# Kernel optimization log

Measured on AMD Instinct MI355X. Metric: run time of the kernel, lower is better.

Reference implementation:

```python
import jax, jax.numpy as jnp
import numpy as np

D = 1024
H = 16
HD = D // H
EPS = 1e-5


def layer_norm(x, g, b):
    mu = jnp.mean(x, axis=-1, keepdims=True)
    var = jnp.mean((x - mu) ** 2, axis=-1, keepdims=True)
    return (x - mu) * jax.lax.rsqrt(var + EPS) * g + b


def setup_inputs() -> dict:
    key = jax.random.key(0)
    ks = jax.random.split(key, 10)
    s = lambda fan_in: 1.0 / np.sqrt(fan_in)
    inp = {
        "x": jax.random.normal(ks[0], (2, 2048, D), dtype=jnp.float32),
        "w_qkv": jax.random.uniform(ks[1], (D, 3 * D), minval=-s(D), maxval=s(D)),
        "b_qkv": jnp.zeros((3 * D,), jnp.float32),
        "w_fc": jax.random.uniform(ks[2], (D, D), minval=-s(D), maxval=s(D)),
        "b_fc": jnp.zeros((D,), jnp.float32),
        "ln1_g": jnp.ones((D,), jnp.float32),
        "ln1_b": jnp.zeros((D,), jnp.float32),
        "ln2_g": jnp.ones((D,), jnp.float32),
        "ln2_b": jnp.zeros((D,), jnp.float32),
        "w1": jax.random.uniform(ks[3], (D, 4 * D), minval=-s(D), maxval=s(D)),
        "b1": jnp.zeros((4 * D,), jnp.float32),
        "w2": jax.random.uniform(ks[4], (4 * D, D), minval=-s(4 * D), maxval=s(4 * D)),
        "b2": jnp.zeros((D,), jnp.float32),
    }
    return inp


def reference(x, w_qkv, b_qkv, w_fc, b_fc, ln1_g, ln1_b, ln2_g, ln2_b, w1, b1, w2, b2):
    B, T, C = x.shape
    # --- attention sublayer (pre-norm) ---
    h = layer_norm(x, ln1_g, ln1_b)
    qkv = (h @ w_qkv + b_qkv).reshape(B, T, 3, H, HD)
    q, k, v = qkv[:, :, 0], qkv[:, :, 1], qkv[:, :, 2]  # [B,T,H,HD]
    scores = jnp.einsum("bqhd,bkhd->bhqk", q, k) / np.sqrt(HD).astype(np.float32)
    causal = jnp.tril(jnp.ones((T, T), dtype=bool))
    scores = jnp.where(causal, scores, -jnp.inf)
    weights = jax.nn.softmax(scores, axis=-1)
    out = jnp.einsum("bhqk,bkhd->bqhd", weights, v).reshape(B, T, C)
    x = x + out @ w_fc + b_fc
    # --- MLP sublayer (pre-norm) ---
    h = layer_norm(x, ln2_g, ln2_b)
    h = jax.nn.gelu(h @ w1 + b1, approximate=False) @ w2 + b2
    return x + h
```

## Files before the change

kernel.cpp:

```cpp
#include <hip/hip_runtime.h>
#include <hip/hip_bf16.h>
#include <cstdint>
#include <cstddef>

#define SEQ 2048
#define DM  1024

typedef __attribute__((ext_vector_type(8))) __bf16 bf16x8;
typedef __attribute__((ext_vector_type(4))) float  f32x4;
using bf16 = __hip_bfloat16;

__device__ __forceinline__ void gload_lds16(const bf16* g, bf16* l) {
  __builtin_amdgcn_global_load_lds((const __attribute__((address_space(1))) void*)g,
                                   (__attribute__((address_space(3))) void*)l,
                                   16, 0, 0);
}

__global__ void transpose_to_bf16(const float* __restrict__ in, bf16* __restrict__ out,
                                  int K, int N) {
  __shared__ float tile[32][33];
  const int k0 = blockIdx.y * 32, n0 = blockIdx.x * 32;
  const int tx = threadIdx.x, ty = threadIdx.y;
#pragma unroll
  for (int i = ty; i < 32; i += 8)
    tile[i][tx] = in[(size_t)(k0 + i) * N + n0 + tx];
  __syncthreads();
#pragma unroll
  for (int i = ty; i < 32; i += 8)
    out[(size_t)(n0 + i) * K + k0 + tx] = __float2bfloat16(tile[tx][i]);
}

__global__ void ln_to_bf16(const float* __restrict__ x, const float* __restrict__ g,
                           const float* __restrict__ bt, bf16* __restrict__ out) {
  const int row = blockIdx.x;
  const float4 v = ((const float4*)(x + (size_t)row * DM))[threadIdx.x];
  float s  = v.x + v.y + v.z + v.w;
  float s2 = v.x * v.x + v.y * v.y + v.z * v.z + v.w * v.w;
#pragma unroll
  for (int o = 32; o > 0; o >>= 1) { s += __shfl_down(s, o); s2 += __shfl_down(s2, o); }
  __shared__ float red[8];
  const int wave = threadIdx.x >> 6, lane = threadIdx.x & 63;
  if (lane == 0) { red[wave] = s; red[4 + wave] = s2; }
  __syncthreads();
  s  = red[0] + red[1] + red[2] + red[3];
  s2 = red[4] + red[5] + red[6] + red[7];
  const float mu  = s * (1.f / DM);
  const float var = s2 * (1.f / DM) - mu * mu;
  const float r   = rsqrtf(var + 1e-5f);
  const float4 gv = ((const float4*)g)[threadIdx.x];
  const float4 bv = ((const float4*)bt)[threadIdx.x];
  bf16* o = out + (size_t)row * DM + threadIdx.x * 4;
  o[0] = __float2bfloat16((v.x - mu) * r * gv.x + bv.x);
  o[1] = __float2bfloat16((v.y - mu) * r * gv.y + bv.y);
  o[2] = __float2bfloat16((v.z - mu) * r * gv.z + bv.z);
  o[3] = __float2bfloat16((v.w - mu) * r * gv.w + bv.w);
}

enum { EP_BF16 = 0, EP_GELU = 1, EP_RESID = 2 };

template <int MODE>
__global__ void gemm_bt(const bf16* __restrict__ A, const bf16* __restrict__ Bt,
                        const float* __restrict__ bias, const float* __restrict__ resid,
                        float* __restrict__ Cf, bf16* __restrict__ Cb,
                        int M, int N, int K) {
  __shared__ __attribute__((aligned(16))) bf16 As[128 * 32];
  __shared__ __attribute__((aligned(16))) bf16 Bs[128 * 32];
  const int tid  = threadIdx.x;
  const int wave = tid >> 6, lane = tid & 63;
  const int l16 = lane & 15, lq = lane >> 4;
  const int m0 = blockIdx.x * 128, n0 = blockIdx.y * 128;
  const int wr = (wave >> 1) * 64, wc = (wave & 1) * 64;

  f32x4 acc[4][4];
#pragma unroll
  for (int i = 0; i < 4; i++)
#pragma unroll
    for (int j = 0; j < 4; j++) acc[i][j] = 0;

  const int srow = tid >> 2;
  const int scol = (tid & 3) * 8;
  const bf16* ga = A  + (size_t)(m0 + srow) * K + scol;
  const bf16* gb = Bt + (size_t)(n0 + srow) * K + scol;
  bf16* la = As + (size_t)wave * 512;
  bf16* lb = Bs + (size_t)wave * 512;

  for (int kt = 0; kt < K; kt += 32) {
    gload_lds16(ga + kt, la);
    gload_lds16(ga + (size_t)64 * K + kt, la + 2048);
    gload_lds16(gb + kt, lb);
    gload_lds16(gb + (size_t)64 * K + kt, lb + 2048);
    __syncthreads();
    bf16x8 af[4], bfr[4];
#pragma unroll
    for (int mi = 0; mi < 4; mi++)
      af[mi] = *(const bf16x8*)(As + (wr + mi * 16 + l16) * 32 + lq * 8);
#pragma unroll
    for (int ni = 0; ni < 4; ni++)
      bfr[ni] = *(const bf16x8*)(Bs + (wc + ni * 16 + l16) * 32 + lq * 8);
#pragma unroll
    for (int mi = 0; mi < 4; mi++)
#pragma unroll
      for (int ni = 0; ni < 4; ni++)
        acc[mi][ni] = __builtin_amdgcn_mfma_f32_16x16x32_bf16(af[mi], bfr[ni], acc[mi][ni], 0, 0, 0);
    __syncthreads();
  }

#pragma unroll
  for (int ni = 0; ni < 4; ni++) {
    const int col = n0 + wc + ni * 16 + l16;
    const float bb = bias[col];
#pragma unroll
    for (int mi = 0; mi < 4; mi++) {
#pragma unroll
      for (int r = 0; r < 4; r++) {
        const int row = m0 + wr + mi * 16 + lq * 4 + r;
        const size_t idx = (size_t)row * N + col;
        float v = acc[mi][ni][r] + bb;
        if (MODE == EP_BF16) {
          Cb[idx] = __float2bfloat16(v);
        } else if (MODE == EP_GELU) {
          v = 0.5f * v * (1.0f + erff(v * 0.70710678118654752f));
          Cb[idx] = __float2bfloat16(v);
        } else {
          Cf[idx] = resid[idx] + v;
        }
      }
    }
  }
}

#define SCALE_LOG2 0.18033688011112042f

__global__ void flash_attn(const bf16* __restrict__ qkv, bf16* __restrict__ out) {
  const int id = blockIdx.x;
  const int a  = id & 7;
  const int h  = (id >> 3) & 15;
  const int b  = (id >> 7) & 1;
  const int m  = (id >> 8) & 3;
  const int qb = a ^ (((m & 1) * 15) | ((m & 2) << 3));

  const int tid = threadIdx.x;
  const int w = tid >> 6, lane = tid & 63;
  const int l16 = lane & 15, lq = lane >> 4;

  const size_t base = (size_t)b * SEQ * 3072;
  const bf16* Qg = qkv + base + (size_t)h * 64;
  const bf16* Kg = qkv + base + 1024 + (size_t)h * 64;
  const ushort* Vg = (const ushort*)(qkv + base + 2048 + (size_t)h * 64);

  __shared__ __attribute__((aligned(16))) bf16 Qs[64][72];
  __shared__ __attribute__((aligned(16))) bf16 Ks[64][72];
  __shared__ __attribute__((aligned(16))) bf16 VTs[64 * 64];
  __shared__ __attribute__((aligned(16))) bf16 Ps[4][16][72];

  const int q0 = qb * 64;
  const int nkb = qb + 1;

  const int krow = tid >> 2, kcol = (tid & 3) * 16;
  const int vd = tid & 63, vc = tid >> 6;
  const int vsw0 = ((vc ^ (vd & 7)) * 8);
  const int vsw1 = (((vc + 4) ^ (vd & 7)) * 8);

  {
    const int r = tid >> 2, c = (tid & 3) * 16;
    const bf16* src = Qg + (size_t)(q0 + r) * 3072 + c;
    *(uint4*)(&Qs[r][c])     = *(const uint4*)(src);
    *(uint4*)(&Qs[r][c + 8]) = *(const uint4*)(src + 8);

    const bf16* ks = Kg + (size_t)krow * 3072 + kcol;
    const uint4 k0 = *(const uint4*)(ks);
    const uint4 k1 = *(const uint4*)(ks + 8);
    ushort va[8], vb[8];
#pragma unroll
    for (int j = 0; j < 8; j++) va[j] = Vg[(size_t)(vc * 8 + j) * 3072 + vd];
#pragma unroll
    for (int j = 0; j < 8; j++) vb[j] = Vg[(size_t)((vc + 4) * 8 + j) * 3072 + vd];
    *(uint4*)(&Ks[krow][kcol])     = k0;
    *(uint4*)(&Ks[krow][kcol + 8]) = k1;
    uint4 wa, wb;
    wa.x = (uint)va[0] | ((uint)va[1] << 16); wa.y = (uint)va[2] | ((uint)va[3] << 16);
    wa.z = (uint)va[4] | ((uint)va[5] << 16); wa.w = (uint)va[6] | ((uint)va[7] << 16);
    wb.x = (uint)vb[0] | ((uint)vb[1] << 16); wb.y = (uint)vb[2] | ((uint)vb[3] << 16);
    wb.z = (uint)vb[4] | ((uint)vb[5] << 16); wb.w = (uint)vb[6] | ((uint)vb[7] << 16);
    *(uint4*)(&VTs[vd * 64 + vsw0]) = wa;
    *(uint4*)(&VTs[vd * 64 + vsw1]) = wb;
  }
  __syncthreads();

  const bf16x8 qf0 = *(const bf16x8*)(&Qs[w * 16 + l16][lq * 8]);
  const bf16x8 qf1 = *(const bf16x8*)(&Qs[w * 16 + l16][32 + lq * 8]);

  f32x4 oacc[4];
#pragma unroll
  for (int i = 0; i < 4; i++) oacc[i] = 0;
  float lsum[4] = {0.f, 0.f, 0.f, 0.f};

  uint4 kr0, kr1;
  ushort va[8], vb[8];
  const int sw0 = (lq ^ (l16 & 7)) * 8;
  const int sw1 = ((4 + lq) ^ (l16 & 7)) * 8;

  for (int kb = 0; kb < nkb; ++kb) {
    const bool more = (kb + 1 < nkb);

    if (more) {
      const size_t koff = (size_t)((kb + 1) * 64);
      const bf16* ks = Kg + (koff + krow) * 3072 + kcol;
      kr0 = *(const uint4*)(ks);
      kr1 = *(const uint4*)(ks + 8);
#pragma unroll
      for (int j = 0; j < 8; j++) va[j] = Vg[(koff + vc * 8 + j) * 3072 + vd];
#pragma unroll
      for (int j = 0; j < 8; j++) vb[j] = Vg[(koff + (vc + 4) * 8 + j) * 3072 + vd];
    }

    f32x4 sacc[4];
#pragma unroll
    for (int nt = 0; nt < 4; nt++) sacc[nt] = 0;
#pragma unroll
    for (int nt = 0; nt < 4; nt++) {
      const bf16x8 kf0 = *(const bf16x8*)(&Ks[nt * 16 + l16][lq * 8]);
      const bf16x8 kf1 = *(const bf16x8*)(&Ks[nt * 16 + l16][32 + lq * 8]);
      sacc[nt] = __builtin_amdgcn_mfma_f32_16x16x32_bf16(qf0, kf0, sacc[nt], 0, 0, 0);
      sacc[nt] = __builtin_amdgcn_mfma_f32_16x16x32_bf16(qf1, kf1, sacc[nt], 0, 0, 0);
    }

    const bool diag = (kb == qb);
#pragma unroll
    for (int r = 0; r < 4; r++) {
      float e[4];
#pragma unroll
      for (int nt = 0; nt < 4; nt++) {
        float sv = sacc[nt][r] * SCALE_LOG2;
        sv = fminf(sv, 88.f);
        if (diag && (nt * 16 + l16 > w * 16 + lq * 4 + r)) sv = -1e30f;
        e[nt] = exp2f(sv);
        Ps[w][lq * 4 + r][nt * 16 + l16] = __float2bfloat16(e[nt]);
      }
      lsum[r] += (e[0] + e[1]) + (e[2] + e[3]);
    }

    const bf16x8 pf0 = *(const bf16x8*)(&Ps[w][l16][lq * 8]);
    const bf16x8 pf1 = *(const bf16x8*)(&Ps[w][l16][32 + lq * 8]);
#pragma unroll
    for (int dt = 0; dt < 4; dt++) {
      const int d = dt * 16 + l16;
      const bf16x8 vf0 = *(const bf16x8*)(&VTs[d * 64 + sw0]);
      const bf16x8 vf1 = *(const bf16x8*)(&VTs[d * 64 + sw1]);
      oacc[dt] = __builtin_amdgcn_mfma_f32_16x16x32_bf16(pf0, vf0, oacc[dt], 0, 0, 0);
      oacc[dt] = __builtin_amdgcn_mfma_f32_16x16x32_bf16(pf1, vf1, oacc[dt], 0, 0, 0);
    }

    if (more) {
      __syncthreads();
      *(uint4*)(&Ks[krow][kcol])     = kr0;
      *(uint4*)(&Ks[krow][kcol + 8]) = kr1;
      uint4 wa, wb;
      wa.x = (uint)va[0] | ((uint)va[1] << 16); wa.y = (uint)va[2] | ((uint)va[3] << 16);
      wa.z = (uint)va[4] | ((uint)va[5] << 16); wa.w = (uint)va[6] | ((uint)va[7] << 16);
      wb.x = (uint)vb[0] | ((uint)vb[1] << 16); wb.y = (uint)vb[2] | ((uint)vb[3] << 16);
      wb.z = (uint)vb[4] | ((uint)vb[5] << 16); wb.w = (uint)vb[6] | ((uint)vb[7] << 16);
      *(uint4*)(&VTs[vd * 64 + vsw0]) = wa;
      *(uint4*)(&VTs[vd * 64 + vsw1]) = wb;
      __syncthreads();
    }
  }

#pragma unroll
  for (int r = 0; r < 4; r++) {
    float l = lsum[r];
    l += __shfl_xor(l, 1);
    l += __shfl_xor(l, 2);
    l += __shfl_xor(l, 4);
    l += __shfl_xor(l, 8);
    lsum[r] = 1.f / l;
  }
#pragma unroll
  for (int dt = 0; dt < 4; dt++)
#pragma unroll
    for (int r = 0; r < 4; r++) {
      const int qrow = q0 + w * 16 + lq * 4 + r;
      const float v = oacc[dt][r] * lsum[r];
      out[(size_t)(b * SEQ + qrow) * DM + h * 64 + dt * 16 + l16] = __float2bfloat16(v);
    }
}

extern "C" void kernel_launch(void* const* d_in, const int* in_sizes, int n_in,
                              void* d_out, int out_size, void* d_ws, size_t ws_size,
                              hipStream_t stream) {
  const float* x     = (const float*)d_in[0];
  const float* w_qkv = (const float*)d_in[1];
  const float* b_qkv = (const float*)d_in[2];
  const float* w_fc  = (const float*)d_in[3];
  const float* b_fc  = (const float*)d_in[4];
  const float* ln1_g = (const float*)d_in[5];
  const float* ln1_b = (const float*)d_in[6];
  const float* ln2_g = (const float*)d_in[7];
  const float* ln2_b = (const float*)d_in[8];
  const float* w1    = (const float*)d_in[9];
  const float* b1    = (const float*)d_in[10];
  const float* w2    = (const float*)d_in[11];
  const float* b2    = (const float*)d_in[12];
  float* out = (float*)d_out;

  char* ws    = (char*)d_ws;
  float* x2   = (float*)(ws);
  bf16* big   = (bf16*)(ws + (size_t)(16 << 20));
  bf16* small = (bf16*)(ws + (size_t)(48 << 20));
  bf16* wT    = (bf16*)(ws + (size_t)(56 << 20));

  const dim3 tb(32, 8);

  ln_to_bf16<<<dim3(4096), dim3(256), 0, stream>>>(x, ln1_g, ln1_b, small);
  transpose_to_bf16<<<dim3(96, 32), tb, 0, stream>>>(w_qkv, wT, 1024, 3072);
  gemm_bt<EP_BF16><<<dim3(32, 24), dim3(256), 0, stream>>>(
      small, wT, b_qkv, nullptr, nullptr, big, 4096, 3072, 1024);
  flash_attn<<<dim3(1024), dim3(256), 0, stream>>>(big, small);
  transpose_to_bf16<<<dim3(32, 32), tb, 0, stream>>>(w_fc, wT, 1024, 1024);
  gemm_bt<EP_RESID><<<dim3(32, 8), dim3(256), 0, stream>>>(
      small, wT, b_fc, x, x2, nullptr, 4096, 1024, 1024);
  ln_to_bf16<<<dim3(4096), dim3(256), 0, stream>>>(x2, ln2_g, ln2_b, small);
  transpose_to_bf16<<<dim3(128, 32), tb, 0, stream>>>(w1, wT, 1024, 4096);
  gemm_bt<EP_GELU><<<dim3(32, 32), dim3(256), 0, stream>>>(
      small, wT, b1, nullptr, nullptr, big, 4096, 4096, 1024);
  transpose_to_bf16<<<dim3(32, 128), tb, 0, stream>>>(w2, wT, 4096, 1024);
  gemm_bt<EP_RESID><<<dim3(32, 8), dim3(256), 0, stream>>>(
      big, wT, b2, x2, out, nullptr, 4096, 1024, 4096);
}
```

Before: 412.1 us.

## Register-prefetch GEMM tiles with double-buffered swizzled LDS and one barrier

Replaces the direct global-to-LDS loads in the bf16 GEMM with register prefetch three k-tiles ahead, written into a double-buffered LDS tile. The LDS layout gets an XOR swizzle to reduce bank conflicts on the MFMA fragment reads, and the per-iteration barrier count drops from two to one. The aim is to hide global memory latency behind MFMA work. In exchange it uses more registers (16 uint4 prefetch slots) and twice the LDS, which may lower occupancy.

```diff
diff --git a/kernel.cpp b/kernel.cpp
--- a/kernel.cpp
+++ b/kernel.cpp
@@ -8,13 +8,8 @@
 
 typedef __attribute__((ext_vector_type(8))) __bf16 bf16x8;
 typedef __attribute__((ext_vector_type(4))) float  f32x4;
+using bfl6_dummy = int;
 using bf16 = __hip_bfloat16;
-
-__device__ __forceinline__ void gload_lds16(const bf16* g, bf16* l) {
-  __builtin_amdgcn_global_load_lds((const __attribute__((address_space(1))) void*)g,
-                                   (__attribute__((address_space(3))) void*)l,
-                                   16, 0, 0);
-}
 
 __global__ void transpose_to_bf16(const float* __restrict__ in, bf16* __restrict__ out,
                                   int K, int N) {
@@ -63,8 +58,9 @@
                         const float* __restrict__ bias, const float* __restrict__ resid,
                         float* __restrict__ Cf, bf16* __restrict__ Cb,
                         int M, int N, int K) {
-  __shared__ __attribute__((aligned(16))) bf16 As[128 * 32];
-  __shared__ __attribute__((aligned(16))) bf16 Bs[128 * 32];
+  constexpr int BUF = 128 * 32;
+  __shared__ __attribute__((aligned(16))) bf16 As[2 * BUF];
+  __shared__ __attribute__((aligned(16))) bf16 Bs[2 * BUF];
   const int tid  = threadIdx.x;
   const int wave = tid >> 6, lane = tid & 63;
   const int l16 = lane & 15, lq = lane >> 4;
@@ -78,31 +74,69 @@
     for (int j = 0; j < 4; j++) acc[i][j] = 0;
 
   const int srow = tid >> 2;
-  const int scol = (tid & 3) * 8;
-  const bf16* ga = A  + (size_t)(m0 + srow) * K + scol;
-  const bf16* gb = Bt + (size_t)(n0 + srow) * K + scol;
-  bf16* la = As + (size_t)wave * 512;
-  bf16* lb = Bs + (size_t)wave * 512;
-
-  for (int kt = 0; kt < K; kt += 32) {
-    gload_lds16(ga + kt, la);
-    gload_lds16(ga + (size_t)64 * K + kt, la + 2048);
-    gload_lds16(gb + kt, lb);
-    gload_lds16(gb + (size_t)64 * K + kt, lb + 2048);
+  const int sc   = tid & 3;
+  const int scs  = sc ^ ((srow >> 1) & 3);
+  const bf16* ga = A  + (size_t)(m0 + srow) * K + scs * 8;
+  const bf16* gb = Bt + (size_t)(n0 + srow) * K + scs * 8;
+  const int lw = srow * 32 + sc * 8;
+
+  uint4 pa0[4], pa1[4], pb0[4], pb1[4];
+  const int NKT = K >> 5;
+#pragma unroll
+  for (int p = 0; p < 3; p++) {
+    const int kt = p << 5;
+    pa0[p] = *(const uint4*)(ga + kt);
+    pa1[p] = *(const uint4*)(ga + (size_t)64 * K + kt);
+    pb0[p] = *(const uint4*)(gb + kt);
+    pb1[p] = *(const uint4*)(gb + (size_t)64 * K + kt);
+  }
+  *(uint4*)(As + lw)        = pa0[0];
+  *(uint4*)(As + 2048 + lw) = pa1[0];
+  *(uint4*)(Bs + lw)        = pb0[0];
+  *(uint4*)(Bs + 2048 + lw) = pb1[0];
+
+  int racol[4], rbcol[4];
+#pragma unroll
+  for (int i = 0; i < 4; i++) {
+    const int ra = wr + i * 16 + l16;
+    racol[i] = ra * 32 + (lq ^ ((ra >> 1) & 3)) * 8;
+    const int rb = wc + i * 16 + l16;
+    rbcol[i] = rb * 32 + (lq ^ ((rb >> 1) & 3)) * 8;
+  }
+
+#pragma unroll 4
+  for (int it = 0; it < NKT; ++it) {
     __syncthreads();
+    const int cur = it & 1;
+    if (it + 1 < NKT) {
+      const int s = (it + 1) & 3;
+      bf16* Ad = As + (cur ^ 1) * BUF + lw;
+      bf16* Bd = Bs + (cur ^ 1) * BUF + lw;
+      *(uint4*)(Ad)        = pa0[s];
+      *(uint4*)(Ad + 2048) = pa1[s];
+      *(uint4*)(Bd)        = pb0[s];
+      *(uint4*)(Bd + 2048) = pb1[s];
+    }
+    if (it + 3 < NKT) {
+      const int s = (it + 3) & 3;
+      const int kt = (it + 3) << 5;
+      pa0[s] = *(const uint4*)(ga + kt);
+      pa1[s] = *(const uint4*)(ga + (size_t)64 * K + kt);
+      pb0[s] = *(const uint4*)(gb + kt);
+      pb1[s] = *(const uint4*)(gb + (size_t)64 * K + kt);
+    }
     bf16x8 af[4], bfr[4];
 #pragma unroll
     for (int mi = 0; mi < 4; mi++)
-      af[mi] = *(const bf16x8*)(As + (wr + mi * 16 + l16) * 32 + lq * 8);
+      af[mi] = *(const bf16x8*)(As + cur * BUF + racol[mi]);
 #pragma unroll
     for (int ni = 0; ni < 4; ni++)
-      bfr[ni] = *(const bf16x8*)(Bs + (wc + ni * 16 + l16) * 32 + lq * 8);
+      bfr[ni] = *(const bf16x8*)(Bs + cur * BUF + rbcol[ni]);
 #pragma unroll
     for (int mi = 0; mi < 4; mi++)
 #pragma unroll
       for (int ni = 0; ni < 4; ni++)
         acc[mi][ni] = __builtin_amdgcn_mfma_f32_16x16x32_bf16(af[mi], bfr[ni], acc[mi][ni], 0, 0, 0);
-    __syncthreads();
   }
 
 #pragma unroll
```

After: 752.8 us. 1.83x slower.
